# Kernel tuning notes

Measured on AMD Instinct MI355X. Metric: run time of the kernel, lower is better.

The kernel has to match this reference:

```python
import jax, jax.numpy as jnp
import numpy as np

V = 32000      # vocab_size
D = 768        # embed_dim / d_model
NL = 2         # attn_layers
BATCH = 2
T = 1024       # seq_len
ED = 2 * D     # d_inner (expand_factor=2)
NS = 16        # d_state
K = 4          # d_conv
DT_RANK = (D + 15) // 16  # ceil(d_model/16) = 48


def setup_inputs():
    key = jax.random.key(0)
    ks = jax.random.split(key, 12)
    nrm = lambda k, shp, s=0.02: (jax.random.normal(k, shp, jnp.float32) * s)
    tokens = jax.random.randint(ks[0], (BATCH, T), 0, V)
    embed = nrm(ks[1], (V, D))
    in_proj_w = nrm(ks[2], (NL, 2 * ED, D))
    conv_w = nrm(ks[3], (NL, ED, 1, K), 0.1)   # depthwise conv kernel (O=ED, I/g=1, K)
    conv_b = jnp.zeros((NL, ED), jnp.float32)
    x_proj_w = nrm(ks[4], (NL, DT_RANK + 2 * NS, ED))
    dt_proj_w = nrm(ks[5], (NL, ED, DT_RANK), 0.05)
    dt_proj_b = nrm(ks[6], (NL, ED), 0.05)
    # S4D real init: A = -[1..NS] per channel
    A_log = jnp.log(jnp.broadcast_to(jnp.arange(1, NS + 1, dtype=jnp.float32), (NL, ED, NS)))
    D_param = jnp.ones((NL, ED), jnp.float32)
    out_proj_w = nrm(ks[7], (NL, D, ED))
    ln_w = jnp.ones((NL, D), jnp.float32)
    ln_b = jnp.zeros((NL, D), jnp.float32)
    head_w = nrm(ks[8], (V, D))
    head_b = jnp.zeros((V,), jnp.float32)
    return {"tokens": tokens, "embed": embed, "in_proj_w": in_proj_w,
            "conv_w": conv_w, "conv_b": conv_b, "x_proj_w": x_proj_w,
            "dt_proj_w": dt_proj_w, "dt_proj_b": dt_proj_b, "A_log": A_log,
            "D_param": D_param, "out_proj_w": out_proj_w, "ln_w": ln_w,
            "ln_b": ln_b, "head_w": head_w, "head_b": head_b}


def silu(x):
    return x * jax.nn.sigmoid(x)


def layer_norm(x, w, b, eps=1e-5):
    mu = jnp.mean(x, axis=-1, keepdims=True)
    var = jnp.mean(jnp.square(x - mu), axis=-1, keepdims=True)
    return (x - mu) * jax.lax.rsqrt(var + eps) * w + b


def mamba_block(x, in_w, cw, cb, xp_w, dt_w, dt_b, a_log, d_par, out_w):
    # x: (B, T, D)
    xz = jnp.einsum('btd,ed->bte', x, in_w)           # (B, T, 2*ED)
    xin, z = jnp.split(xz, 2, axis=-1)                 # each (B, T, ED)
    # causal depthwise conv over time
    xc = jnp.transpose(xin, (0, 2, 1))                 # (B, ED, T)
    xc = jax.lax.conv_general_dilated(
        xc, cw, window_strides=(1,), padding=[(K - 1, 0)],
        dimension_numbers=('NCH', 'OIH', 'NCH'), feature_group_count=ED)
    xc = xc + cb[None, :, None]
    xin = silu(jnp.transpose(xc, (0, 2, 1)))           # (B, T, ED)
    # selective SSM
    A = -jnp.exp(a_log)                                # (ED, NS)
    dbc = jnp.einsum('bte,fe->btf', xin, xp_w)         # (B, T, dt_rank + 2*NS)
    delta = dbc[..., :DT_RANK]
    Bm = dbc[..., DT_RANK:DT_RANK + NS]                # (B, T, NS)
    Cm = dbc[..., DT_RANK + NS:]                       # (B, T, NS)
    delta = jax.nn.softplus(jnp.einsum('btr,er->bte', delta, dt_w) + dt_b)  # (B, T, ED)
    dA = jnp.exp(delta[..., None] * A)                 # (B, T, ED, NS)
    dBx = (delta * xin)[..., None] * Bm[:, :, None, :] # (B, T, ED, NS)

    def step(h, inp):
        dA_t, dBx_t, C_t = inp                         # (B,ED,NS),(B,ED,NS),(B,NS)
        h = dA_t * h + dBx_t
        y = jnp.einsum('ben,bn->be', h, C_t)
        return h, y

    h0 = jnp.zeros((x.shape[0], ED, NS), xin.dtype)
    _, ys = jax.lax.scan(step, h0,
                         (jnp.swapaxes(dA, 0, 1), jnp.swapaxes(dBx, 0, 1),
                          jnp.swapaxes(Cm, 0, 1)))
    y = jnp.swapaxes(ys, 0, 1) + d_par * xin           # (B, T, ED)
    return jnp.einsum('bte,de->btd', y * silu(z), out_w)


def reference(tokens, embed, in_proj_w, conv_w, conv_b, x_proj_w, dt_proj_w,
              dt_proj_b, A_log, D_param, out_proj_w, ln_w, ln_b, head_w, head_b):
    x = embed[tokens]                                  # (B, T, D)
    for l in range(NL):  # note: NO residual, matches x = ln(layer(x))
        x = layer_norm(
            mamba_block(x, in_proj_w[l], conv_w[l], conv_b[l], x_proj_w[l],
                        dt_proj_w[l], dt_proj_b[l], A_log[l], D_param[l],
                        out_proj_w[l]),
            ln_w[l], ln_b[l])
    return jnp.einsum('btd,vd->btv', x, head_w) + head_b
```

## Files before the change

### kernel.cpp

```cpp
#include <hip/hip_runtime.h>
#include <hip/hip_bf16.h>
#include <cstdint>
#include <cstddef>

using u16 = unsigned short;

#define DEV static __device__ __forceinline__

DEV float bf2f(u16 u) {
  unsigned int x = ((unsigned int)u) << 16;
  float f;
  __builtin_memcpy(&f, &x, 4);
  return f;
}

DEV u16 f2bf(float f) {
  unsigned int x;
  __builtin_memcpy(&x, &f, 4);
  unsigned int r = (x + 0x7fffu + ((x >> 16) & 1u)) >> 16;
  return (u16)r;
}

typedef __bf16 bf16x8 __attribute__((ext_vector_type(8)));
typedef float f32x4 __attribute__((ext_vector_type(4)));

DEV f32x4 mfma_bf16(bf16x8 a, bf16x8 b, f32x4 c) {
  return __builtin_amdgcn_mfma_f32_16x16x32_bf16(a, b, c, 0, 0, 0);
}

DEV void async_ld16(const void* g, void* lds) {
  __builtin_amdgcn_global_load_lds((const __attribute__((address_space(1))) void*)g,
                                   (__attribute__((address_space(3))) void*)lds,
                                   16, 0, 0);
}

DEV void hard_barrier() {
  __builtin_amdgcn_sched_barrier(0);
  __builtin_amdgcn_s_barrier();
  __builtin_amdgcn_sched_barrier(0);
}

__global__ __launch_bounds__(256) void k_cvt_all(
    const float* __restrict__ s0, u16* __restrict__ d0, int n0,
    const float* __restrict__ s1, u16* __restrict__ d1, int n1,
    const float* __restrict__ s2, u16* __restrict__ d2, int n2,
    const float* __restrict__ s3, u16* __restrict__ d3, int n3) {
  const int total = n0 + n1 + n2 + n3;
  for (int i = blockIdx.x * 256 + threadIdx.x; i < total; i += gridDim.x * 256) {
    int j = i;
    if (j < n0) { d0[j] = f2bf(s0[j]); continue; }
    j -= n0;
    if (j < n1) { d1[j] = f2bf(s1[j]); continue; }
    j -= n1;
    if (j < n2) { d2[j] = f2bf(s2[j]); continue; }
    j -= n2;
    d3[j] = f2bf(s3[j]);
  }
}

__global__ __launch_bounds__(256) void k_zero(float* __restrict__ p, int n) {
  const int i = blockIdx.x * 256 + threadIdx.x;
  if (i < n) p[i] = 0.f;
}

template <bool BIAS>
__global__ __launch_bounds__(512, 2) void gemm3(
    const u16* __restrict__ A, const u16* __restrict__ Bw,
    float* __restrict__ Cf, const float* __restrict__ bias,
    int M, int N, int K, int K0, int ldc) {
  __shared__ __align__(16) u16 sA[3 * 128 * 64];
  __shared__ __align__(16) u16 sB[3 * 256 * 64];

  const int tid = threadIdx.x;
  const int wave = tid >> 6;
  const int lane = tid & 63;
  const int nwg = gridDim.x;
  const int w = (blockIdx.x & 7) * (nwg >> 3) + (blockIdx.x >> 3);
  const int mBlocks = M >> 7;
  const int mb = w % mBlocks;
  const int nb = w / mBlocks;
  const int mBase = mb * 128;
  const int nBase = nb * 256;
  const int wm = wave >> 2;
  const int wn = wave & 3;

  f32x4 acc[4][4];
#pragma unroll
  for (int i = 0; i < 4; ++i)
#pragma unroll
    for (int j = 0; j < 4; ++j) acc[i][j] = f32x4{0.f, 0.f, 0.f, 0.f};

  const int rl = lane >> 3;
  const int sw = (lane & 7) ^ rl;

  auto stage = [&](int bf, int kt) {
    const int k0 = kt * 64;
    const int ka = k0 + sw * 8;
    const int kb = (k0 >= K0 ? k0 - K0 : k0) + sw * 8;
    u16* dA = sA + bf * (128 * 64);
    u16* dB = sB + bf * (256 * 64);
#pragma unroll
    for (int r = 0; r < 2; ++r) {
      const int row = r * 64 + wave * 8;
      async_ld16(A + (size_t)(mBase + row + rl) * K + ka, dA + row * 64);
    }
#pragma unroll
    for (int r = 0; r < 4; ++r) {
      const int row = r * 64 + wave * 8;
      async_ld16(Bw + (size_t)(nBase + row + rl) * K0 + kb, dB + row * 64);
    }
  };

  const int nt = K >> 6;
  stage(0, 0);
  stage(1, 1);
  asm volatile("s_waitcnt vmcnt(6)" ::: "memory");
  hard_barrier();

  const int rr = lane & 15;
  const int qh = lane >> 4;

  int p = 0, ps = 2;
  for (int t = 0; t < nt; ++t) {
    if (t + 2 < nt) stage(ps, t + 2);
    const u16* bA = sA + p * (128 * 64);
    const u16* bB = sB + p * (256 * 64);
#pragma unroll
    for (int ks = 0; ks < 2; ++ks) {
      const int q = ks * 4 + qh;
      bf16x8 aF[4], bF[4];
#pragma unroll
      for (int i = 0; i < 4; ++i) {
        const int ra = wm * 64 + i * 16 + rr;
        aF[i] = *(const bf16x8*)(bA + ra * 64 + ((q ^ (ra & 7)) << 3));
      }
#pragma unroll
      for (int j = 0; j < 4; ++j) {
        const int rb = wn * 64 + j * 16 + rr;
        bF[j] = *(const bf16x8*)(bB + rb * 64 + ((q ^ (rb & 7)) << 3));
      }
      __builtin_amdgcn_s_setprio(1);
#pragma unroll
      for (int i = 0; i < 4; ++i)
#pragma unroll
        for (int j = 0; j < 4; ++j)
          acc[i][j] = mfma_bf16(aF[i], bF[j], acc[i][j]);
      __builtin_amdgcn_s_setprio(0);
    }
    if (t + 1 < nt) {
      if (t + 3 <= nt) {
        asm volatile("s_waitcnt vmcnt(6)" ::: "memory");
      } else {
        asm volatile("s_waitcnt vmcnt(0)" ::: "memory");
      }
      hard_barrier();
    }
    p = (p == 2) ? 0 : p + 1;
    ps = (ps == 2) ? 0 : ps + 1;
  }

  const int r0 = (lane >> 4) * 4;
  const int cn = lane & 15;
#pragma unroll
  for (int i = 0; i < 4; ++i) {
    const int mm = mBase + wm * 64 + i * 16 + r0;
#pragma unroll
    for (int j = 0; j < 4; ++j) {
      const int nn = nBase + wn * 64 + j * 16 + cn;
      float bv = 0.f;
      if constexpr (BIAS) bv = bias[nn];
#pragma unroll
      for (int r = 0; r < 4; ++r)
        Cf[(size_t)(mm + r) * ldc + nn] = acc[i][j][r] + bv;
    }
  }
}

template <bool BIAS, bool ATOMIC>
__global__ __launch_bounds__(256, 4) void gemm_bt(
    const u16* __restrict__ Ahi, const u16* __restrict__ Bw,
    float* __restrict__ Cf, const float* __restrict__ bias,
    int M, int N, int K, int K0, int ldc, int kChunk) {
  __shared__ __align__(16) u16 sA[128 * 64];
  __shared__ __align__(16) u16 sB[128 * 64];

  const int tid = threadIdx.x;
  const int wave = tid >> 6;
  const int lane = tid & 63;
  const int mBase = blockIdx.y * 128;
  const int nBase = blockIdx.x * 128;
  const int kBeg = blockIdx.z * kChunk;
  const int wm = wave >> 1;
  const int wn = wave & 1;

  f32x4 acc[4][4];
#pragma unroll
  for (int i = 0; i < 4; ++i)
#pragma unroll
    for (int j = 0; j < 4; ++j) acc[i][j] = f32x4{0.f, 0.f, 0.f, 0.f};

  const int rsub = lane >> 3;
  const int ksub = (lane & 7) * 8;

  for (int k0 = kBeg; k0 < kBeg + kChunk; k0 += 64) {
    const int kb = (k0 >= K0) ? k0 - K0 : k0;
#pragma unroll
    for (int it = 0; it < 4; ++it) {
      const int chunk = it * 4 + wave;
      const int row = chunk * 8 + rsub;
      async_ld16(Ahi + (size_t)(mBase + row) * K + (k0 + ksub), (char*)sA + chunk * 1024);
      int rn = nBase + row;
      if (rn > N - 1) rn = N - 1;
      async_ld16(Bw + (size_t)rn * K0 + (kb + ksub), (char*)sB + chunk * 1024);
    }
    __syncthreads();

    const int rr = lane & 15;
    const int q8 = (lane >> 4) * 8;
#pragma unroll
    for (int ks = 0; ks < 64; ks += 32) {
      bf16x8 aH[4], bF[4];
#pragma unroll
      for (int i = 0; i < 4; ++i) {
        aH[i] = *(const bf16x8*)(sA + (wm * 64 + i * 16 + rr) * 64 + ks + q8);
        bF[i] = *(const bf16x8*)(sB + (wn * 64 + i * 16 + rr) * 64 + ks + q8);
      }
#pragma unroll
      for (int i = 0; i < 4; ++i)
#pragma unroll
        for (int j = 0; j < 4; ++j)
          acc[i][j] = mfma_bf16(aH[i], bF[j], acc[i][j]);
    }
    __syncthreads();
  }

  const int r0 = (lane >> 4) * 4;
  const int cn = lane & 15;
#pragma unroll
  for (int i = 0; i < 4; ++i) {
    const int mm = mBase + wm * 64 + i * 16 + r0;
#pragma unroll
    for (int j = 0; j < 4; ++j) {
      const int nn = nBase + wn * 64 + j * 16 + cn;
      if (nn < N) {
        float bv = 0.f;
        if constexpr (BIAS) bv = bias[nn];
#pragma unroll
        for (int r = 0; r < 4; ++r) {
          if constexpr (ATOMIC)
            atomicAdd(&Cf[(size_t)(mm + r) * ldc + nn], acc[i][j][r]);
          else
            Cf[(size_t)(mm + r) * ldc + nn] = acc[i][j][r] + bv;
        }
      }
    }
  }
}

__global__ __launch_bounds__(256) void k_embed(const int* __restrict__ tok,
                                               const float* __restrict__ emb,
                                               u16* __restrict__ xhl) {
  const int m = blockIdx.x;
  const float* src = emb + (size_t)tok[m] * 768;
  for (int d = threadIdx.x; d < 768; d += 256) {
    const float v = src[d];
    const u16 h = f2bf(v);
    xhl[(size_t)m * 1536 + d] = h;
    xhl[(size_t)m * 1536 + 768 + d] = f2bf(v - bf2f(h));
  }
}

__global__ __launch_bounds__(256) void k_conv(const float* __restrict__ xz,
                                              const float* __restrict__ cw,
                                              const float* __restrict__ cb,
                                              float* __restrict__ xinc,
                                              u16* __restrict__ xihl) {
  const int idx = blockIdx.x * 256 + threadIdx.x;
  const int e = idx % 1536;
  const int m = idx / 1536;
  const int t = m & 1023;
  const int b = m >> 10;
  float acc = cb[e];
#pragma unroll
  for (int k = 0; k < 4; ++k) {
    const int tt = t - 3 + k;
    if (tt >= 0) acc += xz[(size_t)((b << 10) + tt) * 3072 + e] * cw[e * 4 + k];
  }
  const float s = acc / (1.f + __expf(-acc));
  xinc[idx] = s;
  const u16 h = f2bf(s);
  xihl[(size_t)m * 3072 + e] = h;
  xihl[(size_t)m * 3072 + 1536 + e] = f2bf(s - bf2f(h));
}

__global__ __launch_bounds__(256) void k_dt(const float* __restrict__ dbc,
                                            const float* __restrict__ dtw,
                                            const float* __restrict__ dtb,
                                            float* __restrict__ delta) {
  const int m = blockIdx.x;
  __shared__ float sd[48];
  if (threadIdx.x < 48) sd[threadIdx.x] = dbc[m * 80 + threadIdx.x];
  __syncthreads();
  for (int e = threadIdx.x; e < 1536; e += 256) {
    float acc = dtb[e];
#pragma unroll
    for (int r = 0; r < 48; ++r) acc += sd[r] * dtw[e * 48 + r];
    const float sp = (acc > 20.f) ? acc : log1pf(__expf(acc));
    delta[m * 1536 + e] = sp;
  }
}

#define SCAN_NC 16
#define SCAN_CL 64

__global__ __launch_bounds__(256) void k_scan1(
    const float* __restrict__ delta, const float* __restrict__ xinc,
    const float* __restrict__ dbc, const float* __restrict__ alog,
    float* __restrict__ chP, float* __restrict__ chQ) {
  const int b = blockIdx.y;
  const int c = blockIdx.z;
  const int e = blockIdx.x * 16 + (threadIdx.x >> 4);
  const int n = threadIdx.x & 15;
  const float Aen = -__expf(alog[e * 16 + n]);
  const int m0 = (b << 10) + c * SCAN_CL;
  float h = 0.f, P = 1.f;
  float dl = delta[m0 * 1536 + e];
  float xi = xinc[m0 * 1536 + e];
  float Bn = dbc[m0 * 80 + 48 + n];
  for (int t = 0; t < SCAN_CL; ++t) {
    const float dl_c = dl, xi_c = xi, Bn_c = Bn;
    if (t < SCAN_CL - 1) {
      const int m2 = m0 + t + 1;
      dl = delta[m2 * 1536 + e];
      xi = xinc[m2 * 1536 + e];
      Bn = dbc[m2 * 80 + 48 + n];
    }
    const float dA = __expf(dl_c * Aen);
    P *= dA;
    h = dA * h + (dl_c * xi_c) * Bn_c;
  }
  const size_t idx = (((size_t)b * SCAN_NC + c) * 1536 + e) * 16 + n;
  chP[idx] = P;
  chQ[idx] = h;
}

__global__ __launch_bounds__(256) void k_scan_fix(const float* __restrict__ chP,
                                                  const float* __restrict__ chQ,
                                                  float* __restrict__ hst) {
  const int b = blockIdx.y;
  const int e = blockIdx.x * 16 + (threadIdx.x >> 4);
  const int n = threadIdx.x & 15;
  float h = 0.f;
#pragma unroll
  for (int c = 0; c < SCAN_NC; ++c) {
    const size_t idx = (((size_t)b * SCAN_NC + c) * 1536 + e) * 16 + n;
    hst[idx] = h;
    h = chP[idx] * h + chQ[idx];
  }
}

__global__ __launch_bounds__(256) void k_scan2(
    const float* __restrict__ delta, const float* __restrict__ xinc,
    const float* __restrict__ dbc, const float* __restrict__ xz,
    const float* __restrict__ alog, const float* __restrict__ dpar,
    const float* __restrict__ hst, u16* __restrict__ ymhl) {
  const int b = blockIdx.y;
  const int c = blockIdx.z;
  const int e = blockIdx.x * 16 + (threadIdx.x >> 4);
  const int n = threadIdx.x & 15;
  const float Aen = -__expf(alog[e * 16 + n]);
  const float dp = dpar[e];
  const int m0 = (b << 10) + c * SCAN_CL;
  float h = hst[(((size_t)b * SCAN_NC + c) * 1536 + e) * 16 + n];
  float dl = delta[m0 * 1536 + e];
  float xi = xinc[m0 * 1536 + e];
  float Bn = dbc[m0 * 80 + 48 + n];
  float Cn = dbc[m0 * 80 + 64 + n];
  float zz = xz[(size_t)m0 * 3072 + 1536 + e];
  for (int t = 0; t < SCAN_CL; ++t) {
    const float dl_c = dl, xi_c = xi, Bn_c = Bn, Cn_c = Cn, zz_c = zz;
    if (t < SCAN_CL - 1) {
      const int m2 = m0 + t + 1;
      dl = delta[m2 * 1536 + e];
      xi = xinc[m2 * 1536 + e];
      Bn = dbc[m2 * 80 + 48 + n];
      Cn = dbc[m2 * 80 + 64 + n];
      zz = xz[(size_t)m2 * 3072 + 1536 + e];
    }
    const float dA = __expf(dl_c * Aen);
    h = dA * h + (dl_c * xi_c) * Bn_c;
    float p = h * Cn_c;
    p += __shfl_xor(p, 1);
    p += __shfl_xor(p, 2);
    p += __shfl_xor(p, 4);
    p += __shfl_xor(p, 8);
    if (n == 0) {
      const float y = p + dp * xi_c;
      const float sz = zz_c / (1.f + __expf(-zz_c));
      const float ym = y * sz;
      const int mt = m0 + t;
      const u16 hh = f2bf(ym);
      ymhl[(size_t)mt * 3072 + e] = hh;
      ymhl[(size_t)mt * 3072 + 1536 + e] = f2bf(ym - bf2f(hh));
    }
  }
}

__global__ __launch_bounds__(256) void k_ln(const float* __restrict__ g,
                                            const float* __restrict__ w,
                                            const float* __restrict__ bb,
                                            u16* __restrict__ xhl) {
  const int m = blockIdx.x;
  const float* row = g + (size_t)m * 768;
  const int tid = threadIdx.x;
  const float v0 = row[tid], v1 = row[tid + 256], v2 = row[tid + 512];
  float s = v0 + v1 + v2;
#pragma unroll
  for (int o = 32; o > 0; o >>= 1) s += __shfl_xor(s, o);
  __shared__ float red[4];
  if ((tid & 63) == 0) red[tid >> 6] = s;
  __syncthreads();
  const float mu = (red[0] + red[1] + red[2] + red[3]) * (1.f / 768.f);
  const float d0 = v0 - mu, d1 = v1 - mu, d2 = v2 - mu;
  float q = d0 * d0 + d1 * d1 + d2 * d2;
#pragma unroll
  for (int o = 32; o > 0; o >>= 1) q += __shfl_xor(q, o);
  __syncthreads();
  if ((tid & 63) == 0) red[tid >> 6] = q;
  __syncthreads();
  const float var = (red[0] + red[1] + red[2] + red[3]) * (1.f / 768.f);
  const float rs = rsqrtf(var + 1e-5f);
  const float dd[3] = {d0, d1, d2};
#pragma unroll
  for (int i = 0; i < 3; ++i) {
    const int d = tid + i * 256;
    const float y = dd[i] * rs * w[d] + bb[d];
    const u16 h = f2bf(y);
    xhl[(size_t)m * 1536 + d] = h;
    xhl[(size_t)m * 1536 + 768 + d] = f2bf(y - bf2f(h));
  }
}

extern "C" void kernel_launch(void* const* d_in, const int* in_sizes, int n_in,
                              void* d_out, int out_size, void* d_ws, size_t ws_size,
                              hipStream_t stream) {
  const int* tokens = (const int*)d_in[0];
  const float* embed = (const float*)d_in[1];
  const float* in_w = (const float*)d_in[2];
  const float* conv_w = (const float*)d_in[3];
  const float* conv_b = (const float*)d_in[4];
  const float* xp_w = (const float*)d_in[5];
  const float* dt_w = (const float*)d_in[6];
  const float* dt_b = (const float*)d_in[7];
  const float* A_log = (const float*)d_in[8];
  const float* D_par = (const float*)d_in[9];
  const float* out_w = (const float*)d_in[10];
  const float* ln_w = (const float*)d_in[11];
  const float* ln_b = (const float*)d_in[12];
  const float* head_w = (const float*)d_in[13];
  const float* head_b = (const float*)d_in[14];

  char* p = (char*)d_ws;
  auto alloc = [&](size_t bytes) {
    char* r = p;
    p += (bytes + 255) & ~(size_t)255;
    return r;
  };
  float* xz = (float*)alloc(2048ull * 3072 * 4);
  float* xinc = (float*)alloc(2048ull * 1536 * 4);
  u16* xihl = (u16*)alloc(2048ull * 3072 * 2);
  float* dbc = (float*)alloc(2048ull * 80 * 4);
  float* delta = (float*)alloc(2048ull * 1536 * 4);
  u16* ymhl = (u16*)alloc(2048ull * 3072 * 2);
  float* gout = (float*)alloc(2048ull * 768 * 4);
  u16* xhl = (u16*)alloc(2048ull * 1536 * 2);
  u16* w_in_h = (u16*)alloc(2ull * 3072 * 768 * 2);
  u16* w_xp_h = (u16*)alloc(2ull * 80 * 1536 * 2);
  u16* w_out_h = (u16*)alloc(2ull * 768 * 1536 * 2);
  u16* w_head_h = (u16*)alloc(32000ull * 768 * 2);
  float* chP = (float*)alloc(2ull * SCAN_NC * 1536 * 16 * 4);
  float* chQ = (float*)alloc(2ull * SCAN_NC * 1536 * 16 * 4);
  float* hst = (float*)alloc(2ull * SCAN_NC * 1536 * 16 * 4);

  k_cvt_all<<<4096, 256, 0, stream>>>(in_w, w_in_h, 2 * 3072 * 768,
                                      xp_w, w_xp_h, 2 * 80 * 1536,
                                      out_w, w_out_h, 2 * 768 * 1536,
                                      head_w, w_head_h, 32000 * 768);

  k_embed<<<2048, 256, 0, stream>>>(tokens, embed, xhl);

  for (int l = 0; l < 2; ++l) {
    gemm3<false><<<192, 512, 0, stream>>>(
        xhl, w_in_h + (size_t)l * 2359296, xz, nullptr, 2048, 3072, 1536, 768, 3072);

    k_conv<<<12288, 256, 0, stream>>>(xz, conv_w + l * 6144, conv_b + l * 1536, xinc, xihl);

    k_zero<<<640, 256, 0, stream>>>(dbc, 2048 * 80);
    gemm_bt<false, true><<<dim3(1, 16, 12), 256, 0, stream>>>(
        xihl, w_xp_h + (size_t)l * 122880, dbc, nullptr, 2048, 80, 3072, 1536, 80, 256);

    k_dt<<<2048, 256, 0, stream>>>(dbc, dt_w + (size_t)l * 73728, dt_b + l * 1536, delta);

    k_scan1<<<dim3(96, 2, SCAN_NC), 256, 0, stream>>>(
        delta, xinc, dbc, A_log + l * 24576, chP, chQ);
    k_scan_fix<<<dim3(96, 2), 256, 0, stream>>>(chP, chQ, hst);
    k_scan2<<<dim3(96, 2, SCAN_NC), 256, 0, stream>>>(
        delta, xinc, dbc, xz, A_log + l * 24576, D_par + l * 1536, hst, ymhl);

    k_zero<<<6144, 256, 0, stream>>>(gout, 2048 * 768);
    gemm_bt<false, true><<<dim3(6, 16, 8), 256, 0, stream>>>(
        ymhl, w_out_h + (size_t)l * 1179648, gout, nullptr, 2048, 768, 3072, 1536, 768, 384);

    k_ln<<<2048, 256, 0, stream>>>(gout, ln_w + l * 768, ln_b + l * 768, xhl);
  }

  gemm3<true><<<2000, 512, 0, stream>>>(
      xhl, w_head_h, (float*)d_out, head_b, 2048, 32000, 1536, 768, 32000);
}
```

Baseline: 1.348 ms.

## Replace triple-buffered 128x256 GEMM with single-buffer 128x128 tiles, vectorize conversions, transpose dt weights

Replaces the 512-thread, 128x256-tile, triple-buffered async GEMM with a 256-thread 128x128-tile kernel. It loads each K-step into a single LDS buffer between two __syncthreads, doubling the grid and allowing more blocks per CU. It also vectorizes the fp32-to-bf16 weight conversion and the embedding split with float4 loads. It pre-transposes dt_proj weights so k_dt reads them coalesced. Dropping the software pipeline exposes global load latency in the dominant head and in_proj GEMMs, relying on occupancy to hide it instead.

```diff
diff --git a/kernel.cpp b/kernel.cpp
--- a/kernel.cpp
+++ b/kernel.cpp
@@ -23,6 +23,7 @@
 
 typedef __bf16 bf16x8 __attribute__((ext_vector_type(8)));
 typedef float f32x4 __attribute__((ext_vector_type(4)));
+typedef unsigned short u16x4 __attribute__((ext_vector_type(4)));
 
 DEV f32x4 mfma_bf16(bf16x8 a, bf16x8 b, f32x4 c) {
   return __builtin_amdgcn_mfma_f32_16x16x32_bf16(a, b, c, 0, 0, 0);
@@ -32,12 +33,6 @@
   __builtin_amdgcn_global_load_lds((const __attribute__((address_space(1))) void*)g,
                                    (__attribute__((address_space(3))) void*)lds,
                                    16, 0, 0);
-}
-
-DEV void hard_barrier() {
-  __builtin_amdgcn_sched_barrier(0);
-  __builtin_amdgcn_s_barrier();
-  __builtin_amdgcn_sched_barrier(0);
 }
 
 __global__ __launch_bounds__(256) void k_cvt_all(
@@ -45,16 +40,47 @@
     const float* __restrict__ s1, u16* __restrict__ d1, int n1,
     const float* __restrict__ s2, u16* __restrict__ d2, int n2,
     const float* __restrict__ s3, u16* __restrict__ d3, int n3) {
-  const int total = n0 + n1 + n2 + n3;
+  const int t0 = n0 >> 2, t1 = n1 >> 2, t2 = n2 >> 2, t3 = n3 >> 2;
+  const int total = t0 + t1 + t2 + t3;
   for (int i = blockIdx.x * 256 + threadIdx.x; i < total; i += gridDim.x * 256) {
     int j = i;
-    if (j < n0) { d0[j] = f2bf(s0[j]); continue; }
-    j -= n0;
-    if (j < n1) { d1[j] = f2bf(s1[j]); continue; }
-    j -= n1;
-    if (j < n2) { d2[j] = f2bf(s2[j]); continue; }
-    j -= n2;
-    d3[j] = f2bf(s3[j]);
+    const float* s;
+    u16* d;
+    if (j < t0) {
+      s = s0; d = d0;
+    } else {
+      j -= t0;
+      if (j < t1) {
+        s = s1; d = d1;
+      } else {
+        j -= t1;
+        if (j < t2) {
+          s = s2; d = d2;
+        } else {
+          j -= t2;
+          s = s3; d = d3;
+        }
+      }
+    }
+    const float4 v = *(const float4*)(s + 4 * (size_t)j);
+    u16x4 o;
+    o.x = f2bf(v.x);
+    o.y = f2bf(v.y);
+    o.z = f2bf(v.z);
+    o.w = f2bf(v.w);
+    *(u16x4*)(d + 4 * (size_t)j) = o;
+  }
+}
+
+__global__ __launch_bounds__(256) void k_dtt(const float* __restrict__ src,
+                                             float* __restrict__ dst) {
+  const int i = blockIdx.x * 256 + threadIdx.x;
+  if (i < 2 * 48 * 1536) {
+    const int l = i / 73728;
+    const int j = i % 73728;
+    const int r = j / 1536;
+    const int e = j % 1536;
+    dst[i] = src[l * 73728 + e * 48 + r];
   }
 }
 
@@ -64,12 +90,12 @@
 }
 
 template <bool BIAS>
-__global__ __launch_bounds__(512, 2) void gemm3(
+__global__ __launch_bounds__(256, 4) void gemm4(
     const u16* __restrict__ A, const u16* __restrict__ Bw,
     float* __restrict__ Cf, const float* __restrict__ bias,
     int M, int N, int K, int K0, int ldc) {
-  __shared__ __align__(16) u16 sA[3 * 128 * 64];
-  __shared__ __align__(16) u16 sB[3 * 256 * 64];
+  __shared__ __align__(16) u16 sA[128 * 64];
+  __shared__ __align__(16) u16 sB[128 * 64];
 
   const int tid = threadIdx.x;
   const int wave = tid >> 6;
@@ -80,9 +106,9 @@
   const int mb = w % mBlocks;
   const int nb = w / mBlocks;
   const int mBase = mb * 128;
-  const int nBase = nb * 256;
-  const int wm = wave >> 2;
-  const int wn = wave & 3;
+  const int nBase = nb * 128;
+  const int wm = wave >> 1;
+  const int wn = wave & 1;
 
   f32x4 acc[4][4];
 #pragma unroll
@@ -90,41 +116,23 @@
 #pragma unroll
     for (int j = 0; j < 4; ++j) acc[i][j] = f32x4{0.f, 0.f, 0.f, 0.f};
 
-  const int rl = lane >> 3;
-  const int sw = (lane & 7) ^ rl;
-
-  auto stage = [&](int bf, int kt) {
-    const int k0 = kt * 64;
-    const int ka = k0 + sw * 8;
-    const int kb = (k0 >= K0 ? k0 - K0 : k0) + sw * 8;
-    u16* dA = sA + bf * (128 * 64);
-    u16* dB = sB + bf * (256 * 64);
-#pragma unroll
-    for (int r = 0; r < 2; ++r) {
-      const int row = r * 64 + wave * 8;
-      async_ld16(A + (size_t)(mBase + row + rl) * K + ka, dA + row * 64);
-    }
-#pragma unroll
-    for (int r = 0; r < 4; ++r) {
-      const int row = r * 64 + wave * 8;
-      async_ld16(Bw + (size_t)(nBase + row + rl) * K0 + kb, dB + row * 64);
-    }
-  };
-
-  const int nt = K >> 6;
-  stage(0, 0);
-  stage(1, 1);
-  asm volatile("s_waitcnt vmcnt(6)" ::: "memory");
-  hard_barrier();
+  const int rsub = lane >> 3;
+  const int ksub = ((lane & 7) ^ rsub) * 8;
 
   const int rr = lane & 15;
   const int qh = lane >> 4;
 
-  int p = 0, ps = 2;
-  for (int t = 0; t < nt; ++t) {
-    if (t + 2 < nt) stage(ps, t + 2);
-    const u16* bA = sA + p * (128 * 64);
-    const u16* bB = sB + p * (256 * 64);
+  for (int k0 = 0; k0 < K; k0 += 64) {
+    const int kb = (k0 >= K0 ? k0 - K0 : k0);
+#pragma unroll
+    for (int it = 0; it < 4; ++it) {
+      const int chunk = it * 4 + wave;
+      const int row = chunk * 8 + rsub;
+      async_ld16(A + (size_t)(mBase + row) * K + (k0 + ksub), (char*)sA + chunk * 1024);
+      async_ld16(Bw + (size_t)(nBase + row) * K0 + (kb + ksub), (char*)sB + chunk * 1024);
+    }
+    __syncthreads();
+
 #pragma unroll
     for (int ks = 0; ks < 2; ++ks) {
       const int q = ks * 4 + qh;
@@ -132,12 +140,9 @@
 #pragma unroll
       for (int i = 0; i < 4; ++i) {
         const int ra = wm * 64 + i * 16 + rr;
-        aF[i] = *(const bf16x8*)(bA + ra * 64 + ((q ^ (ra & 7)) << 3));
-      }
-#pragma unroll
-      for (int j = 0; j < 4; ++j) {
-        const int rb = wn * 64 + j * 16 + rr;
-        bF[j] = *(const bf16x8*)(bB + rb * 64 + ((q ^ (rb & 7)) << 3));
+        aF[i] = *(const bf16x8*)(sA + ra * 64 + ((q ^ (ra & 7)) << 3));
+        const int rb = wn * 64 + i * 16 + rr;
+        bF[i] = *(const bf16x8*)(sB + rb * 64 + ((q ^ (rb & 7)) << 3));
       }
       __builtin_amdgcn_s_setprio(1);
 #pragma unroll
@@ -147,16 +152,7 @@
           acc[i][j] = mfma_bf16(aF[i], bF[j], acc[i][j]);
       __builtin_amdgcn_s_setprio(0);
     }
-    if (t + 1 < nt) {
-      if (t + 3 <= nt) {
-        asm volatile("s_waitcnt vmcnt(6)" ::: "memory");
-      } else {
-        asm volatile("s_waitcnt vmcnt(0)" ::: "memory");
-      }
-      hard_barrier();
-    }
-    p = (p == 2) ? 0 : p + 1;
-    ps = (ps == 2) ? 0 : ps + 1;
+    __syncthreads();
   }
 
   const int r0 = (lane >> 4) * 4;
@@ -167,11 +163,13 @@
 #pragma unroll
     for (int j = 0; j < 4; ++j) {
       const int nn = nBase + wn * 64 + j * 16 + cn;
-      float bv = 0.f;
-      if constexpr (BIAS) bv = bias[nn];
-#pragma unroll
-      for (int r = 0; r < 4; ++r)
-        Cf[(size_t)(mm + r) * ldc + nn] = acc[i][j][r] + bv;
+      if (nn < N) {
+        float bv = 0.f;
+        if constexpr (BIAS) bv = bias[nn];
+#pragma unroll
+        for (int r = 0; r < 4; ++r)
+          Cf[(size_t)(mm + r) * ldc + nn] = acc[i][j][r] + bv;
+      }
     }
   }
 }
@@ -262,11 +260,17 @@
                                                u16* __restrict__ xhl) {
   const int m = blockIdx.x;
   const float* src = emb + (size_t)tok[m] * 768;
-  for (int d = threadIdx.x; d < 768; d += 256) {
-    const float v = src[d];
-    const u16 h = f2bf(v);
-    xhl[(size_t)m * 1536 + d] = h;
-    xhl[(size_t)m * 1536 + 768 + d] = f2bf(v - bf2f(h));
+  const int d4 = threadIdx.x;
+  if (d4 < 192) {
+    const float4 v = *(const float4*)(src + d4 * 4);
+    u16x4 h, lo;
+    h.x = f2bf(v.x); h.y = f2bf(v.y); h.z = f2bf(v.z); h.w = f2bf(v.w);
+    lo.x = f2bf(v.x - bf2f(h.x));
+    lo.y = f2bf(v.y - bf2f(h.y));
+    lo.z = f2bf(v.z - bf2f(h.z));
+    lo.w = f2bf(v.w - bf2f(h.w));
+    *(u16x4*)(xhl + (size_t)m * 1536 + d4 * 4) = h;
+    *(u16x4*)(xhl + (size_t)m * 1536 + 768 + d4 * 4) = lo;
   }
 }
 
@@ -294,7 +298,7 @@
 }
 
 __global__ __launch_bounds__(256) void k_dt(const float* __restrict__ dbc,
-                                            const float* __restrict__ dtw,
+                                            const float* __restrict__ dtwT,
                                             const float* __restrict__ dtb,
                                             float* __restrict__ delta) {
   const int m = blockIdx.x;
@@ -304,7 +308,7 @@
   for (int e = threadIdx.x; e < 1536; e += 256) {
     float acc = dtb[e];
 #pragma unroll
-    for (int r = 0; r < 48; ++r) acc += sd[r] * dtw[e * 48 + r];
+    for (int r = 0; r < 48; ++r) acc += sd[r] * dtwT[r * 1536 + e];
     const float sp = (acc > 20.f) ? acc : log1pf(__expf(acc));
     delta[m * 1536 + e] = sp;
   }
@@ -478,19 +482,21 @@
   u16* w_xp_h = (u16*)alloc(2ull * 80 * 1536 * 2);
   u16* w_out_h = (u16*)alloc(2ull * 768 * 1536 * 2);
   u16* w_head_h = (u16*)alloc(32000ull * 768 * 2);
+  float* dtwT = (float*)alloc(2ull * 48 * 1536 * 4);
   float* chP = (float*)alloc(2ull * SCAN_NC * 1536 * 16 * 4);
   float* chQ = (float*)alloc(2ull * SCAN_NC * 1536 * 16 * 4);
   float* hst = (float*)alloc(2ull * SCAN_NC * 1536 * 16 * 4);
 
-  k_cvt_all<<<4096, 256, 0, stream>>>(in_w, w_in_h, 2 * 3072 * 768,
+  k_cvt_all<<<2048, 256, 0, stream>>>(in_w, w_in_h, 2 * 3072 * 768,
                                       xp_w, w_xp_h, 2 * 80 * 1536,
                                       out_w, w_out_h, 2 * 768 * 1536,
                                       head_w, w_head_h, 32000 * 768);
+  k_dtt<<<576, 256, 0, stream>>>(dt_w, dtwT);
 
   k_embed<<<2048, 256, 0, stream>>>(tokens, embed, xhl);
 
   for (int l = 0; l < 2; ++l) {
-    gemm3<false><<<192, 512, 0, stream>>>(
+    gemm4<false><<<384, 256, 0, stream>>>(
         xhl, w_in_h + (size_t)l * 2359296, xz, nullptr, 2048, 3072, 1536, 768, 3072);
 
     k_conv<<<12288, 256, 0, stream>>>(xz, conv_w + l * 6144, conv_b + l * 1536, xinc, xihl);
@@ -499,7 +505,7 @@
     gemm_bt<false, true><<<dim3(1, 16, 12), 256, 0, stream>>>(
         xihl, w_xp_h + (size_t)l * 122880, dbc, nullptr, 2048, 80, 3072, 1536, 80, 256);
 
-    k_dt<<<2048, 256, 0, stream>>>(dbc, dt_w + (size_t)l * 73728, dt_b + l * 1536, delta);
+    k_dt<<<2048, 256, 0, stream>>>(dbc, dtwT + (size_t)l * 73728, dt_b + l * 1536, delta);
 
     k_scan1<<<dim3(96, 2, SCAN_NC), 256, 0, stream>>>(
         delta, xinc, dbc, A_log + l * 24576, chP, chQ);
@@ -514,6 +520,6 @@
     k_ln<<<2048, 256, 0, stream>>>(gout, ln_w + l * 768, ln_b + l * 768, xhl);
   }
 
-  gemm3<true><<<2000, 512, 0, stream>>>(
+  gemm4<true><<<4000, 256, 0, stream>>>(
       xhl, w_head_h, (float*)d_out, head_b, 2048, 32000, 1536, 768, 32000);
 }
```

Result: faster. 1.216 ms (-9.8%).
